# Kernel tuning notes

Hardware: AMD Instinct MI355X
Metric: run time of the kernel (lower is better)

Reference implementation:

```python
import math
import jax, jax.numpy as jnp
import numpy as np

B, C, H, W = 8, 512, 32, 32
N_HEADS = 8
N_GROUPS = 32  # GroupNorm(32) as in guided-diffusion normalization()
EPS = 1e-5


def setup_inputs() -> dict:
    key = jax.random.key(0)
    k0, k1, k2, k3, k4 = jax.random.split(key, 5)
    x = jax.random.normal(k0, (B, C, H, W), dtype=jnp.float32)
    gn_scale = jnp.ones((C,), dtype=jnp.float32)
    gn_bias = jnp.zeros((C,), dtype=jnp.float32)
    # 1x1 conv weights stored as (out, in); proj_out is zero-initialized in the
    # original but we use small random weights so the op is non-trivial.
    qkv_w = jax.random.normal(k1, (3 * C, C), dtype=jnp.float32) * 0.02
    qkv_b = jax.random.normal(k2, (3 * C,), dtype=jnp.float32) * 0.02
    proj_w = jax.random.normal(k3, (C, C), dtype=jnp.float32) * 0.02
    proj_b = jax.random.normal(k4, (C,), dtype=jnp.float32) * 0.02
    return {"x": x, "gn_scale": gn_scale, "gn_bias": gn_bias,
            "qkv_w": qkv_w, "qkv_b": qkv_b, "proj_w": proj_w, "proj_b": proj_b}


def reference(x, gn_scale, gn_bias, qkv_w, qkv_b, proj_w, proj_b):
    b, c, h, w = x.shape
    L = h * w
    xf = x.reshape(b, c, L)

    # GroupNorm(32): normalize over (channels-in-group, length)
    xg = xf.reshape(b, N_GROUPS, c // N_GROUPS, L)
    mu = jnp.mean(xg, axis=(2, 3), keepdims=True)
    var = jnp.var(xg, axis=(2, 3), keepdims=True)
    xn = ((xg - mu) * jax.lax.rsqrt(var + EPS)).reshape(b, c, L)
    xn = xn * gn_scale[None, :, None] + gn_bias[None, :, None]

    # 1x1 conv -> qkv (b, 3c, L)
    qkv = jnp.einsum('oc,bcl->bol', qkv_w, xn) + qkv_b[None, :, None]

    ch = c // N_HEADS  # head dim (width//(3*n_heads) of qkv)
    q, k, v = jnp.split(qkv, 3, axis=1)
    q = q.reshape(b * N_HEADS, ch, L)
    k = k.reshape(b * N_HEADS, ch, L)
    v = v.reshape(b * N_HEADS, ch, L)

    scale = 1.0 / math.sqrt(math.sqrt(ch))
    # scores: (b*heads, L, L) materialized, as in the original
    wts = jnp.einsum('bct,bcs->bts', q * scale, k * scale)
    wts = jax.nn.softmax(wts.astype(jnp.float32), axis=-1).astype(q.dtype)
    a = jnp.einsum('bts,bcs->bct', wts, v).reshape(b, c, L)

    # zero-initialized 1x1 proj in original; random weights here
    hout = jnp.einsum('oc,bcl->bol', proj_w, a) + proj_b[None, :, None]
    return (xf + hout).reshape(b, c, h, w)
```

## Files before the change

kernel.cpp:

```cpp
#include <hip/hip_runtime.h>
#include <math.h>

#define BATCH   8
#define CCH     512
#define LL      1024
#define NHEADS  8
#define CHD     64
#define EPSV    1e-5f
#define QSCALE  0.1803368801111204f

typedef __bf16 bf16_t;
typedef bf16_t bf16x8 __attribute__((ext_vector_type(8)));
typedef bf16_t bf16x4 __attribute__((ext_vector_type(4)));
typedef float  f32x4  __attribute__((ext_vector_type(4)));

__device__ __forceinline__ bf16_t f2b(float f) {
  unsigned u = __float_as_uint(f);
  u += 0x7fff + ((u >> 16) & 1);
  return __builtin_bit_cast(bf16_t, (unsigned short)(u >> 16));
}

__device__ __forceinline__ unsigned pack2(float lo, float hi) {
  unsigned a = (unsigned)__builtin_bit_cast(unsigned short, f2b(lo));
  unsigned b = (unsigned)__builtin_bit_cast(unsigned short, f2b(hi));
  return (b << 16) | a;
}

__device__ __forceinline__ void gload_lds16(const void* g, void* l) {
  __builtin_amdgcn_global_load_lds(
      (const __attribute__((address_space(1))) void*)g,
      (__attribute__((address_space(3))) void*)l, 16, 0, 0);
}

__global__ __launch_bounds__(256) void prep_fused(const float* __restrict__ qkvw,
                                                  const float* __restrict__ projw,
                                                  bf16_t* __restrict__ wqb,
                                                  bf16_t* __restrict__ wpb,
                                                  const float* __restrict__ x,
                                                  const float* __restrict__ gsc,
                                                  const float* __restrict__ gbi,
                                                  bf16_t* __restrict__ xnT) {
  int bid = blockIdx.x;
  int tid = threadIdx.x;
  if (bid < 1024) {
    int i = (bid * 256 + tid) * 4;
    const float* src;
    bf16_t* dst;
    int j;
    if (i < 1536 * 512) { src = qkvw; dst = wqb; j = i; }
    else                { src = projw; dst = wpb; j = i - 1536 * 512; }
    float4 v = *(const float4*)(src + j);
    bf16x4 o = {f2b(v.x), f2b(v.y), f2b(v.z), f2b(v.w)};
    *(bf16x4*)(dst + j) = o;
    return;
  }
  int lin = bid - 1024;
  int xcd = lin & 7, slot = lin >> 3;
  int b = slot & 7, jj = slot >> 3;
  int g = xcd * 4 + jj;
  const float4* x4 = (const float4*)(x + ((size_t)(b * 32 + g)) * 16 * LL);

  float s = 0.f, ss = 0.f;
  float4 v[16];
#pragma unroll
  for (int it = 0; it < 16; ++it) {
    float4 f = x4[it * 256 + tid];
    v[it] = f;
    s += f.x + f.y + f.z + f.w;
    ss += f.x * f.x + f.y * f.y + f.z * f.z + f.w * f.w;
  }
#pragma unroll
  for (int m = 1; m < 64; m <<= 1) { s += __shfl_xor(s, m); ss += __shfl_xor(ss, m); }
  __shared__ float rs_[4], rss[4];
  int wv = tid >> 6, ln = tid & 63;
  if (ln == 0) { rs_[wv] = s; rss[wv] = ss; }
  __syncthreads();
  s  = rs_[0] + rs_[1] + rs_[2] + rs_[3];
  ss = rss[0] + rss[1] + rss[2] + rss[3];
  float mean = s * (1.f / 16384.f);
  float var  = ss * (1.f / 16384.f) - mean * mean;
  float rstd = rsqrtf(var + EPSV);

  float sc[16], bi[16];
#pragma unroll
  for (int it = 0; it < 16; ++it) {
    sc[it] = gsc[g * 16 + it] * rstd;
    bi[it] = gbi[g * 16 + it] - mean * sc[it];
  }

#pragma unroll
  for (int j = 0; j < 4; ++j) {
    unsigned w[8];
#pragma unroll
    for (int k = 0; k < 8; ++k) {
      float a0 = (j == 0 ? v[2 * k].x : j == 1 ? v[2 * k].y : j == 2 ? v[2 * k].z : v[2 * k].w);
      float a1 = (j == 0 ? v[2 * k + 1].x : j == 1 ? v[2 * k + 1].y : j == 2 ? v[2 * k + 1].z : v[2 * k + 1].w);
      w[k] = pack2(a0 * sc[2 * k] + bi[2 * k], a1 * sc[2 * k + 1] + bi[2 * k + 1]);
    }
    int l = tid * 4 + j;
    bf16_t* dst = xnT + ((size_t)b * LL + l) * CCH + g * 16;
    *(uint4*)dst = make_uint4(w[0], w[1], w[2], w[3]);
    *(uint4*)(dst + 8) = make_uint4(w[4], w[5], w[6], w[7]);
  }
}

__global__ __launch_bounds__(256) void qkv_mfma(const bf16_t* __restrict__ wq,
                                                const bf16_t* __restrict__ xnT,
                                                const float* __restrict__ qkvb,
                                                bf16_t* __restrict__ qt,
                                                bf16_t* __restrict__ kt,
                                                bf16_t* __restrict__ vt) {
  __shared__ bf16_t As[128 * 64];
  __shared__ bf16_t Bs[128 * 64];
  int tid = threadIdx.x;
  int wave = tid >> 6, lane = tid & 63;
  int lrow = lane & 15, quad = lane >> 4;
  int wm = wave >> 1, wn = wave & 1;
  int b = blockIdx.x;
  int oBase = blockIdx.y * 128, lBase = blockIdx.z * 128;
  int srow = lane >> 3;
  int sgOff = (((lane & 7) ^ srow) << 4);

  f32x4 acc[4][4] = {};
  for (int ktile = 0; ktile < 8; ++ktile) {
    int kB = ktile * 64;
    __syncthreads();
#pragma unroll
    for (int j = 0; j < 4; ++j) {
      int ci = wave * 4 + j;
      int R = ci * 8 + srow;
      gload_lds16((const char*)(wq + (size_t)(oBase + R) * CCH + kB) + sgOff,
                  (char*)As + ci * 1024);
      gload_lds16((const char*)(xnT + ((size_t)b * LL + lBase + R) * CCH + kB) + sgOff,
                  (char*)Bs + ci * 1024);
    }
    __syncthreads();
#pragma unroll
    for (int kk = 0; kk < 2; ++kk) {
      bf16x8 af[4], bfr[4];
#pragma unroll
      for (int m = 0; m < 4; ++m) {
        int r = wm * 64 + m * 16 + lrow;
        int g = (kk * 4 + quad) ^ (lrow & 7);
        af[m] = *(const bf16x8*)(As + r * 64 + g * 8);
      }
#pragma unroll
      for (int n = 0; n < 4; ++n) {
        int r = wn * 64 + n * 16 + lrow;
        int g = (kk * 4 + quad) ^ (lrow & 7);
        bfr[n] = *(const bf16x8*)(Bs + r * 64 + g * 8);
      }
#pragma unroll
      for (int m = 0; m < 4; ++m)
#pragma unroll
        for (int n = 0; n < 4; ++n)
          acc[m][n] = __builtin_amdgcn_mfma_f32_16x16x32_bf16(af[m], bfr[n], acc[m][n], 0, 0, 0);
    }
  }

  int oW = oBase + wm * 64;
  int lW = lBase + wn * 64;
  int sec = oW >> 9;
#pragma unroll
  for (int m = 0; m < 4; ++m) {
    int o4 = oW + m * 16 + quad * 4;
    float4 bb4 = *(const float4*)&qkvb[o4];
    int cc = o4 & 511;
    int head = cc >> 6, ch = cc & 63;
    int bh = b * NHEADS + head;
    if (sec == 0) {
#pragma unroll
      for (int n = 0; n < 4; ++n) {
        int l = lW + n * 16 + lrow;
        unsigned d0 = pack2((acc[m][n][0] + bb4.x) * QSCALE,
                            (acc[m][n][1] + bb4.y) * QSCALE);
        unsigned d1 = pack2((acc[m][n][2] + bb4.z) * QSCALE,
                            (acc[m][n][3] + bb4.w) * QSCALE);
        *(uint2*)(qt + ((size_t)bh * LL + l) * CHD + ch) = make_uint2(d0, d1);
      }
    } else if (sec == 1) {
#pragma unroll
      for (int n = 0; n < 4; ++n) {
        int l = lW + n * 16 + lrow;
        unsigned d0 = pack2(acc[m][n][0] + bb4.x, acc[m][n][1] + bb4.y);
        unsigned d1 = pack2(acc[m][n][2] + bb4.z, acc[m][n][3] + bb4.w);
        *(uint2*)(kt + ((size_t)bh * LL + l) * CHD + ch) = make_uint2(d0, d1);
      }
    } else {
      float bb[4] = {bb4.x, bb4.y, bb4.z, bb4.w};
#pragma unroll
      for (int i = 0; i < 4; ++i) {
        unsigned d0 = pack2(acc[m][0][i] + bb[i], acc[m][1][i] + bb[i]);
        unsigned d1 = pack2(acc[m][2][i] + bb[i], acc[m][3][i] + bb[i]);
        *(uint2*)(vt + ((size_t)bh * CHD + ch + i) * LL + lW + lrow * 4) =
            make_uint2(d0, d1);
      }
    }
  }
}

__global__ __launch_bounds__(256) void attn_mfma(const bf16_t* __restrict__ qt,
                                                 const bf16_t* __restrict__ kt,
                                                 const bf16_t* __restrict__ vt,
                                                 bf16_t* __restrict__ at) {
  __shared__ bf16_t kbuf[2][64 * 64];
  __shared__ bf16_t pb[8 * 16 * 72];
  int tid = threadIdx.x, wave = tid >> 6, lane = tid & 63;
  int lrow = lane & 15, quad = lane >> 4;
  int bh = blockIdx.x;
  int tW = blockIdx.y * 128 + wave * 32;
  const bf16_t* qb = qt + (size_t)bh * LL * CHD;
  const bf16_t* kb = kt + (size_t)bh * LL * CHD;
  const bf16_t* vb = vt + (size_t)bh * CHD * LL;

  int srow = lane >> 3;
  int sgb = (((lane & 7) ^ srow) << 4);

  bf16x8 qf[2][2];
#pragma unroll
  for (int h = 0; h < 2; ++h) {
    const bf16_t* qp = qb + (size_t)(tW + h * 16 + lrow) * CHD + quad * 8;
    qf[h][0] = *(const bf16x8*)qp;
    qf[h][1] = *(const bf16x8*)(qp + 32);
  }

  bf16x8 ones;
#pragma unroll
  for (int j = 0; j < 8; ++j) ones[j] = (bf16_t)1.0f;

  f32x4 Oa[2][4] = {};
  f32x4 Os[2] = {};

#pragma unroll
  for (int j = 0; j < 2; ++j) {
    int c = wave * 2 + j;
    int R = c * 8 + srow;
    gload_lds16((const char*)(kb + (size_t)R * CHD) + sgb, (char*)&kbuf[0][0] + c * 1024);
  }
  __syncthreads();

  int swz0 = (quad ^ (lrow & 7)) * 8;
  int swz1 = ((quad + 4) ^ (lrow & 7)) * 8;

  for (int st = 0; st < 16; ++st) {
    int cur = st & 1;
    int sB = st * 64;

    bf16x8 vf0[4], vf1[4];
#pragma unroll
    for (int n = 0; n < 4; ++n) {
      const bf16_t* vp = vb + (size_t)(n * 16 + lrow) * LL + sB + quad * 8;
      vf0[n] = *(const bf16x8*)vp;
      vf1[n] = *(const bf16x8*)(vp + 32);
    }

    if (st < 15) {
      int sBn = sB + 64;
#pragma unroll
      for (int j = 0; j < 2; ++j) {
        int c = wave * 2 + j;
        int R = c * 8 + srow;
        gload_lds16((const char*)(kb + (size_t)(sBn + R) * CHD) + sgb,
                    (char*)&kbuf[cur ^ 1][0] + c * 1024);
      }
    }
    const bf16_t* kbase = &kbuf[cur][0];

    f32x4 S[2][4];
#pragma unroll
    for (int ss = 0; ss < 4; ++ss) {
      int s = ss * 16 + lrow;
      bf16x8 k0 = *(const bf16x8*)(kbase + s * 64 + swz0);
      bf16x8 k1 = *(const bf16x8*)(kbase + s * 64 + swz1);
#pragma unroll
      for (int h = 0; h < 2; ++h) {
        f32x4 z = {0.f, 0.f, 0.f, 0.f};
        z = __builtin_amdgcn_mfma_f32_16x16x32_bf16(qf[h][0], k0, z, 0, 0, 0);
        S[h][ss] = __builtin_amdgcn_mfma_f32_16x16x32_bf16(qf[h][1], k1, z, 0, 0, 0);
      }
    }

#pragma unroll
    for (int h = 0; h < 2; ++h) {
      bf16_t* pw = pb + (wave * 2 + h) * (16 * 72);
      float p[4][4];
#pragma unroll
      for (int ss = 0; ss < 4; ++ss)
#pragma unroll
        for (int i = 0; i < 4; ++i)
          p[ss][i] = __builtin_amdgcn_exp2f(S[h][ss][i]);
#pragma unroll
      for (int i = 0; i < 4; ++i) {
        unsigned d0 = __builtin_amdgcn_perm(__float_as_uint(p[1][i]),
                                            __float_as_uint(p[0][i]), 0x07060302u);
        unsigned d1 = __builtin_amdgcn_perm(__float_as_uint(p[3][i]),
                                            __float_as_uint(p[2][i]), 0x07060302u);
        uint2* dst = (uint2*)(pw + (quad * 4 + i) * 72 + lrow * 4);
        *dst = make_uint2(d0, d1);
      }
    }
    asm volatile("s_waitcnt lgkmcnt(0)" ::: "memory");

    bf16x8 pf[2][2];
#pragma unroll
    for (int h = 0; h < 2; ++h) {
      const bf16_t* pw = pb + (wave * 2 + h) * (16 * 72);
      pf[h][0] = *(const bf16x8*)(pw + lrow * 72 + quad * 8);
      pf[h][1] = *(const bf16x8*)(pw + lrow * 72 + 32 + quad * 8);
    }

#pragma unroll
    for (int n = 0; n < 4; ++n) {
#pragma unroll
      for (int h = 0; h < 2; ++h) {
        Oa[h][n] = __builtin_amdgcn_mfma_f32_16x16x32_bf16(pf[h][0], vf0[n], Oa[h][n], 0, 0, 0);
        Oa[h][n] = __builtin_amdgcn_mfma_f32_16x16x32_bf16(pf[h][1], vf1[n], Oa[h][n], 0, 0, 0);
      }
    }
#pragma unroll
    for (int h = 0; h < 2; ++h) {
      Os[h] = __builtin_amdgcn_mfma_f32_16x16x32_bf16(pf[h][0], ones, Os[h], 0, 0, 0);
      Os[h] = __builtin_amdgcn_mfma_f32_16x16x32_bf16(pf[h][1], ones, Os[h], 0, 0, 0);
    }

    __syncthreads();
  }

  bf16_t* ab = at + (size_t)bh * LL * CHD;
#pragma unroll
  for (int h = 0; h < 2; ++h) {
    float inv[4];
#pragma unroll
    for (int i = 0; i < 4; ++i) inv[i] = 1.f / Os[h][i];
#pragma unroll
    for (int n = 0; n < 4; ++n)
#pragma unroll
      for (int i = 0; i < 4; ++i)
        ab[(size_t)(tW + h * 16 + quad * 4 + i) * CHD + n * 16 + lrow] =
            f2b(Oa[h][n][i] * inv[i]);
  }
}

__global__ __launch_bounds__(256) void proj_mfma(const bf16_t* __restrict__ wp,
                                                 const bf16_t* __restrict__ at,
                                                 const float* __restrict__ projb,
                                                 const float* __restrict__ x,
                                                 float* __restrict__ out) {
  __shared__ bf16_t As[128 * 64];
  __shared__ bf16_t Bs[128 * 64];
  int tid = threadIdx.x;
  int wave = tid >> 6, lane = tid & 63;
  int lrow = lane & 15, quad = lane >> 4;
  int wm = wave >> 1, wn = wave & 1;
  int b = blockIdx.x;
  int oBase = blockIdx.y * 128, lBase = blockIdx.z * 128;
  int srow = lane >> 3;
  int sgOff = (((lane & 7) ^ srow) << 4);

  f32x4 acc[4][4] = {};
  for (int ktile = 0; ktile < 8; ++ktile) {
    int kB = ktile * 64;
    __syncthreads();
#pragma unroll
    for (int j = 0; j < 4; ++j) {
      int ci = wave * 4 + j;
      int R = ci * 8 + srow;
      gload_lds16((const char*)(wp + (size_t)(oBase + R) * CCH + kB) + sgOff,
                  (char*)As + ci * 1024);
      gload_lds16((const char*)(at + ((size_t)(b * NHEADS + ktile) * LL + lBase + R) * CHD) + sgOff,
                  (char*)Bs + ci * 1024);
    }
    __syncthreads();
#pragma unroll
    for (int kk = 0; kk < 2; ++kk) {
      bf16x8 af[4], bfr[4];
#pragma unroll
      for (int m = 0; m < 4; ++m) {
        int r = wm * 64 + m * 16 + lrow;
        int g = (kk * 4 + quad) ^ (lrow & 7);
        af[m] = *(const bf16x8*)(As + r * 64 + g * 8);
      }
#pragma unroll
      for (int n = 0; n < 4; ++n) {
        int r = wn * 64 + n * 16 + lrow;
        int g = (kk * 4 + quad) ^ (lrow & 7);
        bfr[n] = *(const bf16x8*)(Bs + r * 64 + g * 8);
      }
#pragma unroll
      for (int m = 0; m < 4; ++m)
#pragma unroll
        for (int n = 0; n < 4; ++n)
          acc[m][n] = __builtin_amdgcn_mfma_f32_16x16x32_bf16(af[m], bfr[n], acc[m][n], 0, 0, 0);
    }
  }

  int oW = oBase + wm * 64;
  int lW = lBase + wn * 64;
#pragma unroll
  for (int m = 0; m < 4; ++m) {
#pragma unroll
    for (int i = 0; i < 4; ++i) {
      int o = oW + m * 16 + quad * 4 + i;
      float bb = projb[o];
#pragma unroll
      for (int n = 0; n < 4; ++n) {
        int l = lW + n * 16 + lrow;
        size_t off = ((size_t)(b * CCH + o)) * LL + l;
        out[off] = acc[m][n][i] + bb + x[off];
      }
    }
  }
}

extern "C" void kernel_launch(void* const* d_in, const int* in_sizes, int n_in,
                              void* d_out, int out_size, void* d_ws, size_t ws_size,
                              hipStream_t stream) {
  const float* x     = (const float*)d_in[0];
  const float* gsc   = (const float*)d_in[1];
  const float* gbi   = (const float*)d_in[2];
  const float* qkvw  = (const float*)d_in[3];
  const float* qkvb  = (const float*)d_in[4];
  const float* projw = (const float*)d_in[5];
  const float* projb = (const float*)d_in[6];
  float* out = (float*)d_out;

  char* ws = (char*)d_ws;
  bf16_t* wqb   = (bf16_t*)(ws + 4096);
  bf16_t* wpb   = (bf16_t*)(ws + 4096 + 1572864);
  bf16_t* xnT   = (bf16_t*)(ws + 2101248);
  bf16_t* qt    = (bf16_t*)(ws + 2101248 + 8388608);
  bf16_t* kt    = (bf16_t*)(ws + 2101248 + 2 * 8388608);
  bf16_t* vt    = (bf16_t*)(ws + 2101248 + 3 * 8388608);
  bf16_t* at    = (bf16_t*)(ws + 2101248 + 4 * 8388608);

  hipLaunchKernelGGL(prep_fused, dim3(1280), dim3(256), 0, stream,
                     qkvw, projw, wqb, wpb, x, gsc, gbi, xnT);
  hipLaunchKernelGGL(qkv_mfma, dim3(BATCH, 12, 8), dim3(256), 0, stream,
                     wqb, xnT, qkvb, qt, kt, vt);
  hipLaunchKernelGGL(attn_mfma, dim3(64, 8), dim3(256), 0, stream, qt, kt, vt, at);
  hipLaunchKernelGGL(proj_mfma, dim3(BATCH, 4, 8), dim3(256), 0, stream,
                     wpb, at, projb, x, out);
}
```

Baseline: 166.0 us.

## Widen QKV GEMM tile to 128x256 and stage V through LDS in attention

The QKV projection GEMM now computes a 128x256 output tile per block, with each wave holding 4x8 MFMA accumulators. This halves the grid along L and improves reuse of the weight tile. The attention kernel now double-buffers V tiles into LDS with async global-to-LDS loads, alongside K, instead of each wave loading V fragments directly from global memory every step. The costs are higher register pressure and more LDS per block in both kernels, which may reduce occupancy, and fewer blocks in the QKV GEMM.

```diff
diff --git a/kernel.cpp b/kernel.cpp
--- a/kernel.cpp
+++ b/kernel.cpp
@@ -104,24 +104,24 @@
   }
 }
 
-__global__ __launch_bounds__(256) void qkv_mfma(const bf16_t* __restrict__ wq,
-                                                const bf16_t* __restrict__ xnT,
-                                                const float* __restrict__ qkvb,
-                                                bf16_t* __restrict__ qt,
-                                                bf16_t* __restrict__ kt,
-                                                bf16_t* __restrict__ vt) {
+__global__ __launch_bounds__(256, 2) void qkv_mfma(const bf16_t* __restrict__ wq,
+                                                   const bf16_t* __restrict__ xnT,
+                                                   const float* __restrict__ qkvb,
+                                                   bf16_t* __restrict__ qt,
+                                                   bf16_t* __restrict__ kt,
+                                                   bf16_t* __restrict__ vt) {
   __shared__ bf16_t As[128 * 64];
-  __shared__ bf16_t Bs[128 * 64];
+  __shared__ bf16_t Bs[256 * 64];
   int tid = threadIdx.x;
   int wave = tid >> 6, lane = tid & 63;
   int lrow = lane & 15, quad = lane >> 4;
   int wm = wave >> 1, wn = wave & 1;
   int b = blockIdx.x;
-  int oBase = blockIdx.y * 128, lBase = blockIdx.z * 128;
+  int oBase = blockIdx.y * 128, lBase = blockIdx.z * 256;
   int srow = lane >> 3;
   int sgOff = (((lane & 7) ^ srow) << 4);
 
-  f32x4 acc[4][4] = {};
+  f32x4 acc[4][8] = {};
   for (int ktile = 0; ktile < 8; ++ktile) {
     int kB = ktile * 64;
     __syncthreads();
@@ -131,35 +131,39 @@
       int R = ci * 8 + srow;
       gload_lds16((const char*)(wq + (size_t)(oBase + R) * CCH + kB) + sgOff,
                   (char*)As + ci * 1024);
+    }
+#pragma unroll
+    for (int j = 0; j < 8; ++j) {
+      int ci = wave * 8 + j;
+      int R = ci * 8 + srow;
       gload_lds16((const char*)(xnT + ((size_t)b * LL + lBase + R) * CCH + kB) + sgOff,
                   (char*)Bs + ci * 1024);
     }
     __syncthreads();
 #pragma unroll
     for (int kk = 0; kk < 2; ++kk) {
-      bf16x8 af[4], bfr[4];
+      int g = (kk * 4 + quad) ^ (lrow & 7);
+      bf16x8 af[4], bfr[8];
 #pragma unroll
       for (int m = 0; m < 4; ++m) {
         int r = wm * 64 + m * 16 + lrow;
-        int g = (kk * 4 + quad) ^ (lrow & 7);
         af[m] = *(const bf16x8*)(As + r * 64 + g * 8);
       }
 #pragma unroll
-      for (int n = 0; n < 4; ++n) {
-        int r = wn * 64 + n * 16 + lrow;
-        int g = (kk * 4 + quad) ^ (lrow & 7);
+      for (int n = 0; n < 8; ++n) {
+        int r = wn * 128 + n * 16 + lrow;
         bfr[n] = *(const bf16x8*)(Bs + r * 64 + g * 8);
       }
 #pragma unroll
       for (int m = 0; m < 4; ++m)
 #pragma unroll
-        for (int n = 0; n < 4; ++n)
+        for (int n = 0; n < 8; ++n)
           acc[m][n] = __builtin_amdgcn_mfma_f32_16x16x32_bf16(af[m], bfr[n], acc[m][n], 0, 0, 0);
     }
   }
 
   int oW = oBase + wm * 64;
-  int lW = lBase + wn * 64;
+  int lW = lBase + wn * 128;
   int sec = oW >> 9;
 #pragma unroll
   for (int m = 0; m < 4; ++m) {
@@ -170,7 +174,7 @@
     int bh = b * NHEADS + head;
     if (sec == 0) {
 #pragma unroll
-      for (int n = 0; n < 4; ++n) {
+      for (int n = 0; n < 8; ++n) {
         int l = lW + n * 16 + lrow;
         unsigned d0 = pack2((acc[m][n][0] + bb4.x) * QSCALE,
                             (acc[m][n][1] + bb4.y) * QSCALE);
@@ -180,7 +184,7 @@
       }
     } else if (sec == 1) {
 #pragma unroll
-      for (int n = 0; n < 4; ++n) {
+      for (int n = 0; n < 8; ++n) {
         int l = lW + n * 16 + lrow;
         unsigned d0 = pack2(acc[m][n][0] + bb4.x, acc[m][n][1] + bb4.y);
         unsigned d1 = pack2(acc[m][n][2] + bb4.z, acc[m][n][3] + bb4.w);
@@ -189,11 +193,14 @@
     } else {
       float bb[4] = {bb4.x, bb4.y, bb4.z, bb4.w};
 #pragma unroll
-      for (int i = 0; i < 4; ++i) {
-        unsigned d0 = pack2(acc[m][0][i] + bb[i], acc[m][1][i] + bb[i]);
-        unsigned d1 = pack2(acc[m][2][i] + bb[i], acc[m][3][i] + bb[i]);
-        *(uint2*)(vt + ((size_t)bh * CHD + ch + i) * LL + lW + lrow * 4) =
-            make_uint2(d0, d1);
+      for (int c = 0; c < 2; ++c) {
+#pragma unroll
+        for (int i = 0; i < 4; ++i) {
+          unsigned d0 = pack2(acc[m][c * 4 + 0][i] + bb[i], acc[m][c * 4 + 1][i] + bb[i]);
+          unsigned d1 = pack2(acc[m][c * 4 + 2][i] + bb[i], acc[m][c * 4 + 3][i] + bb[i]);
+          *(uint2*)(vt + ((size_t)bh * CHD + ch + i) * LL + lW + c * 64 + lrow * 4) =
+              make_uint2(d0, d1);
+        }
       }
     }
   }
@@ -204,6 +211,7 @@
                                                  const bf16_t* __restrict__ vt,
                                                  bf16_t* __restrict__ at) {
   __shared__ bf16_t kbuf[2][64 * 64];
+  __shared__ bf16_t vbuf[2][64 * 64];
   __shared__ bf16_t pb[8 * 16 * 72];
   int tid = threadIdx.x, wave = tid >> 6, lane = tid & 63;
   int lrow = lane & 15, quad = lane >> 4;
@@ -236,6 +244,7 @@
     int c = wave * 2 + j;
     int R = c * 8 + srow;
     gload_lds16((const char*)(kb + (size_t)R * CHD) + sgb, (char*)&kbuf[0][0] + c * 1024);
+    gload_lds16((const char*)(vb + (size_t)R * LL) + sgb, (char*)&vbuf[0][0] + c * 1024);
   }
   __syncthreads();
 
@@ -244,27 +253,20 @@
 
   for (int st = 0; st < 16; ++st) {
     int cur = st & 1;
-    int sB = st * 64;
-
-    bf16x8 vf0[4], vf1[4];
-#pragma unroll
-    for (int n = 0; n < 4; ++n) {
-      const bf16_t* vp = vb + (size_t)(n * 16 + lrow) * LL + sB + quad * 8;
-      vf0[n] = *(const bf16x8*)vp;
-      vf1[n] = *(const bf16x8*)(vp + 32);
-    }
-
     if (st < 15) {
-      int sBn = sB + 64;
+      int sBn = (st + 1) * 64;
 #pragma unroll
       for (int j = 0; j < 2; ++j) {
         int c = wave * 2 + j;
         int R = c * 8 + srow;
         gload_lds16((const char*)(kb + (size_t)(sBn + R) * CHD) + sgb,
                     (char*)&kbuf[cur ^ 1][0] + c * 1024);
+        gload_lds16((const char*)(vb + (size_t)R * LL + sBn) + sgb,
+                    (char*)&vbuf[cur ^ 1][0] + c * 1024);
       }
     }
     const bf16_t* kbase = &kbuf[cur][0];
+    const bf16_t* vbase = &vbuf[cur][0];
 
     f32x4 S[2][4];
 #pragma unroll
@@ -311,10 +313,13 @@
 
 #pragma unroll
     for (int n = 0; n < 4; ++n) {
+      int r = (n * 16 + lrow) * 64;
+      bf16x8 v0 = *(const bf16x8*)(vbase + r + swz0);
+      bf16x8 v1 = *(const bf16x8*)(vbase + r + swz1);
 #pragma unroll
       for (int h = 0; h < 2; ++h) {
-        Oa[h][n] = __builtin_amdgcn_mfma_f32_16x16x32_bf16(pf[h][0], vf0[n], Oa[h][n], 0, 0, 0);
-        Oa[h][n] = __builtin_amdgcn_mfma_f32_16x16x32_bf16(pf[h][1], vf1[n], Oa[h][n], 0, 0, 0);
+        Oa[h][n] = __builtin_amdgcn_mfma_f32_16x16x32_bf16(pf[h][0], v0, Oa[h][n], 0, 0, 0);
+        Oa[h][n] = __builtin_amdgcn_mfma_f32_16x16x32_bf16(pf[h][1], v1, Oa[h][n], 0, 0, 0);
       }
     }
 #pragma unroll
@@ -373,17 +378,16 @@
     __syncthreads();
 #pragma unroll
     for (int kk = 0; kk < 2; ++kk) {
+      int g = (kk * 4 + quad) ^ (lrow & 7);
       bf16x8 af[4], bfr[4];
 #pragma unroll
       for (int m = 0; m < 4; ++m) {
         int r = wm * 64 + m * 16 + lrow;
-        int g = (kk * 4 + quad) ^ (lrow & 7);
         af[m] = *(const bf16x8*)(As + r * 64 + g * 8);
       }
 #pragma unroll
       for (int n = 0; n < 4; ++n) {
         int r = wn * 64 + n * 16 + lrow;
-        int g = (kk * 4 + quad) ^ (lrow & 7);
         bfr[n] = *(const bf16x8*)(Bs + r * 64 + g * 8);
       }
 #pragma unroll
@@ -435,7 +439,7 @@
 
   hipLaunchKernelGGL(prep_fused, dim3(1280), dim3(256), 0, stream,
                      qkvw, projw, wqb, wpb, x, gsc, gbi, xnT);
-  hipLaunchKernelGGL(qkv_mfma, dim3(BATCH, 12, 8), dim3(256), 0, stream,
+  hipLaunchKernelGGL(qkv_mfma, dim3(BATCH, 12, 4), dim3(256), 0, stream,
                      wqb, xnT, qkvb, qt, kt, vt);
   hipLaunchKernelGGL(attn_mfma, dim3(64, 8), dim3(256), 0, stream, qt, kt, vt, at);
   hipLaunchKernelGGL(proj_mfma, dim3(BATCH, 4, 8), dim3(256), 0, stream,
```

After: 155.3 us. -6.5%, faster.
